# Performance work log

Hardware: AMD Instinct MI355X
Metric: run time of the kernel (lower is better)

The kernel has to match this reference:

```python
import jax, jax.numpy as jnp
import numpy as np

N = 100000      # nodes
E = 1600000     # edges (avg degree 16)
IN = 128        # in_channels
H = 128         # hidden_channels
EPS = 1e-5      # BatchNorm eps


def setup_inputs() -> dict:
    key = jax.random.key(0)
    ks = jax.random.split(key, 10)
    x = jax.random.normal(ks[0], (N, IN), jnp.float32)
    edge_index = jax.random.randint(ks[1], (2, E), 0, N, dtype=jnp.int32)

    def lin(k, i, o):
        return jax.random.normal(k, (i, o), jnp.float32) * (1.0 / np.sqrt(i))

    d2 = 2 * H
    return {
        "x": x, "edge_index": edge_index,
        # SAGEConv 1: 128 -> 128
        "w1l": lin(ks[2], IN, H), "w1r": lin(ks[3], IN, H), "b1": jnp.zeros((H,), jnp.float32),
        "g1": jnp.ones((H,), jnp.float32), "be1": jnp.zeros((H,), jnp.float32),
        "m1": jnp.zeros((H,), jnp.float32), "v1": jnp.ones((H,), jnp.float32),
        # SAGEConv 2: 128 -> 256
        "w2l": lin(ks[4], H, d2), "w2r": lin(ks[5], H, d2), "b2": jnp.zeros((d2,), jnp.float32),
        "g2": jnp.ones((d2,), jnp.float32), "be2": jnp.zeros((d2,), jnp.float32),
        "m2": jnp.zeros((d2,), jnp.float32), "v2": jnp.ones((d2,), jnp.float32),
        # SAGEConv 3: 256 -> 256
        "w3l": lin(ks[6], d2, d2), "w3r": lin(ks[7], d2, d2), "b3": jnp.zeros((d2,), jnp.float32),
        "g3": jnp.ones((d2,), jnp.float32), "be3": jnp.zeros((d2,), jnp.float32),
        "m3": jnp.zeros((d2,), jnp.float32), "v3": jnp.ones((d2,), jnp.float32),
    }


def _sage_conv(x, src, dst, wl, wr, b):
    # PyG SAGEConv (mean aggr): out = mean_{j in N(i)} x_j @ W_l + x_i @ W_r + b
    agg = jax.ops.segment_sum(x[src], dst, num_segments=N)          # [N, d_in]
    deg = jax.ops.segment_sum(jnp.ones((src.shape[0],), x.dtype), dst, num_segments=N)
    mean = agg / jnp.maximum(deg, 1.0)[:, None]
    return mean @ wl + x @ wr + b


def _bn(x, g, b, m, v):
    # BatchNorm1d in eval mode (running stats); dropout is a no-op in eval
    return (x - m) * jax.lax.rsqrt(v + EPS) * g + b


def reference(x, edge_index,
              w1l, w1r, b1, g1, be1, m1, v1,
              w2l, w2r, b2, g2, be2, m2, v2,
              w3l, w3r, b3, g3, be3, m3, v3):
    src, dst = edge_index[0], edge_index[1]
    h = _bn(jax.nn.relu(_sage_conv(x, src, dst, w1l, w1r, b1)), g1, be1, m1, v1)
    h = _bn(jax.nn.relu(_sage_conv(h, src, dst, w2l, w2r, b2)), g2, be2, m2, v2)
    h = _bn(jax.nn.relu(_sage_conv(h, src, dst, w3l, w3r, b3)), g3, be3, m3, v3)
    return h  # [N, 2*H]
```

## Files before the change

### kernel.cpp

```cpp
#include <hip/hip_runtime.h>

#define NNODES 100000
#define NEDGES 1600000
#define EPSV 1e-5f

#define NB   391
#define BCAP 4608
#define EPB  4096

#define PART_BLKS 391
#define CVT_BLKS  12500
#define WT_BLKS   896

typedef __attribute__((ext_vector_type(8))) short bf16x8;
typedef __attribute__((ext_vector_type(4))) float f32x4;
typedef __attribute__((ext_vector_type(2))) float f32x2;

#if defined(__has_builtin)
#  if __has_builtin(__builtin_amdgcn_cvt_pk_f32_fp8) && __has_builtin(__builtin_amdgcn_cvt_pk_fp8_f32)
#    define HAS_FP8_CVT 1
#  endif
#endif
#ifndef HAS_FP8_CVT
#  define HAS_FP8_CVT 0
#endif

__device__ __forceinline__ ushort f2bf(float f) {
    union { float f; uint u; } c; c.f = f;
    uint u = c.u;
    return (ushort)((u + 0x7fffu + ((u >> 16) & 1u)) >> 16);
}
__device__ __forceinline__ uint pack2(float f0, float f1) {
    return (uint)f2bf(f0) | ((uint)f2bf(f1) << 16);
}

#if !HAS_FP8_CVT
__device__ __forceinline__ float fp8_dec1(uint b) {
    uint e = (b >> 3) & 0xFu, m = b & 7u, s = b >> 7;
    union { uint u; float f; } c;
    c.u = e ? ((s << 31) | ((e + 120u) << 23) | (m << 20)) : (s << 31);
    return c.f;
}
__device__ __forceinline__ uint fp8_enc1(float x) {
    union { float f; uint u; } c; c.f = x;
    uint u = c.u, s = u >> 31;
    float ax = fabsf(x);
    if (ax < 0.015625f) return s << 7;
    if (ax > 448.0f)    return (s << 7) | 0x7Eu;
    u = u + 0x7FFFFu + ((u >> 20) & 1u);
    uint e = ((u >> 23) & 0xFFu) - 120u;
    uint m = (u >> 20) & 7u;
    if (e > 15u) return (s << 7) | 0x7Eu;
    return (s << 7) | (e << 3) | m;
}
#endif

__device__ __forceinline__ void accf8p(f32x2* a, uint2 v) {
#if HAS_FP8_CVT
    a[0] += __builtin_amdgcn_cvt_pk_f32_fp8((int)v.x, false);
    a[1] += __builtin_amdgcn_cvt_pk_f32_fp8((int)v.x, true);
    a[2] += __builtin_amdgcn_cvt_pk_f32_fp8((int)v.y, false);
    a[3] += __builtin_amdgcn_cvt_pk_f32_fp8((int)v.y, true);
#else
    a[0] += (f32x2){fp8_dec1(v.x & 0xFFu), fp8_dec1((v.x >> 8) & 0xFFu)};
    a[1] += (f32x2){fp8_dec1((v.x >> 16) & 0xFFu), fp8_dec1(v.x >> 24)};
    a[2] += (f32x2){fp8_dec1(v.y & 0xFFu), fp8_dec1((v.y >> 8) & 0xFFu)};
    a[3] += (f32x2){fp8_dec1((v.y >> 16) & 0xFFu), fp8_dec1(v.y >> 24)};
#endif
}

__device__ __forceinline__ uint f2fp8(float f) {
#if HAS_FP8_CVT
    return ((uint)__builtin_amdgcn_cvt_pk_fp8_f32(f, f, 0, false)) & 0xFFu;
#else
    return fp8_enc1(f);
#endif
}

__device__ __forceinline__ uint packf8_4(float f0, float f1, float f2, float f3) {
#if HAS_FP8_CVT
    int r = 0;
    r = __builtin_amdgcn_cvt_pk_fp8_f32(f0, f1, r, false);
    r = __builtin_amdgcn_cvt_pk_fp8_f32(f2, f3, r, true);
    return (uint)r;
#else
    return fp8_enc1(f0) | (fp8_enc1(f1) << 8) | (fp8_enc1(f2) << 16) | (fp8_enc1(f3) << 24);
#endif
}

__device__ __forceinline__ void load_lds16(const ushort* g, ushort* l) {
    __builtin_amdgcn_global_load_lds(
        (const __attribute__((address_space(1))) void*)g,
        (__attribute__((address_space(3))) void*)l,
        16, 0, 0);
}

__global__ __launch_bounds__(256) void pre_kernel(
    const int* __restrict__ src, const int* __restrict__ dst,
    int* __restrict__ cursor, uint2* __restrict__ pairs, int E,
    const float* __restrict__ x, ushort* __restrict__ xbf,
    unsigned char* __restrict__ xf8, int n4,
    const float* __restrict__ w1l, const float* __restrict__ w1r,
    const float* __restrict__ w2l, const float* __restrict__ w2r,
    const float* __restrict__ w3l, const float* __restrict__ w3r,
    ushort* __restrict__ t1l, ushort* __restrict__ t1r,
    ushort* __restrict__ t2l, ushort* __restrict__ t2r,
    ushort* __restrict__ t3l, ushort* __restrict__ t3r)
{
    const int t = threadIdx.x;

    if (blockIdx.x < PART_BLKS) {
        __shared__ int lcnt[NB];
        __shared__ int lbase[NB];
        for (int i = t; i < NB; i += 256) lcnt[i] = 0;
        __syncthreads();

        const int base = blockIdx.x * EPB;
        const int lim  = min(base + EPB, E);

        for (int e = base + t; e < lim; e += 256)
            atomicAdd(&lcnt[((unsigned)dst[e]) >> 8], 1);
        __syncthreads();

        for (int i = t; i < NB; i += 256) {
            int c = lcnt[i];
            lbase[i] = c ? atomicAdd(&cursor[i], c) : 0;
            lcnt[i] = 0;
        }
        __syncthreads();

        for (int e = base + t; e < lim; e += 256) {
            int d = dst[e];
            int b = ((unsigned)d) >> 8;
            int p = lbase[b] + atomicAdd(&lcnt[b], 1);
            if (p < BCAP) pairs[(size_t)b * BCAP + p] = make_uint2((uint)src[e], (uint)d);
        }
    } else if (blockIdx.x < PART_BLKS + CVT_BLKS) {
        int i = (blockIdx.x - PART_BLKS) * 256 + t;
        if (i < n4) {
            float4 v = ((const float4*)x)[i];
            ushort4 o;
            o.x = f2bf(v.x); o.y = f2bf(v.y); o.z = f2bf(v.z); o.w = f2bf(v.w);
            ((ushort4*)xbf)[i] = o;
            ((uint*)xf8)[i] = packf8_4(v.x, v.y, v.z, v.w);
        }
    } else {
        int idx = (blockIdx.x - PART_BLKS - CVT_BLKS) * 256 + t;
        const float* w; ushort* wt; int K, Nout, i;
        if      (idx <  16384) { w = w1l; wt = t1l; K = 128; Nout = 128; i = idx; }
        else if (idx <  32768) { w = w1r; wt = t1r; K = 128; Nout = 128; i = idx - 16384; }
        else if (idx <  65536) { w = w2l; wt = t2l; K = 128; Nout = 256; i = idx - 32768; }
        else if (idx <  98304) { w = w2r; wt = t2r; K = 128; Nout = 256; i = idx - 65536; }
        else if (idx < 163840) { w = w3l; wt = t3l; K = 256; Nout = 256; i = idx - 98304; }
        else if (idx < 229376) { w = w3r; wt = t3r; K = 256; Nout = 256; i = idx - 163840; }
        else return;
        int k = i / Nout, n = i - k * Nout;
        wt[(size_t)n * K + k] = f2bf(w[i]);
    }
}

__global__ __launch_bounds__(512) void bscan_kernel(const int* __restrict__ cursor,
                                                    int* __restrict__ colBase)
{
    __shared__ int s[512];
    int t = threadIdx.x;
    int v = (t < NB) ? min(cursor[t], BCAP) : 0;
    s[t] = v;
    __syncthreads();
    #pragma unroll
    for (int off = 1; off < 512; off <<= 1) {
        int a = (t >= off) ? s[t - off] : 0;
        __syncthreads();
        s[t] += a;
        __syncthreads();
    }
    if (t < NB) colBase[t] = s[t] - v;
}

__global__ __launch_bounds__(256) void csr_fin_kernel(
    const uint2* __restrict__ pairs, const int* __restrict__ cursor,
    const int* __restrict__ colBase, uint2* __restrict__ meta,
    int* __restrict__ col, int n)
{
    __shared__ int lcnt[256];
    __shared__ int lofs[256];
    const int b = blockIdx.x;
    const int t = threadIdx.x;
    const int ecnt  = min(cursor[b], BCAP);
    const int cbase = colBase[b];
    const uint2* __restrict__ pp = pairs + (size_t)b * BCAP;

    lcnt[t] = 0;
    __syncthreads();
    for (int e = t; e < ecnt; e += 256)
        atomicAdd(&lcnt[pp[e].y & 255u], 1);
    __syncthreads();

    const int v = lcnt[t];
    lofs[t] = v;
    __syncthreads();
    #pragma unroll
    for (int off = 1; off < 256; off <<= 1) {
        int a = (t >= off) ? lofs[t - off] : 0;
        __syncthreads();
        lofs[t] += a;
        __syncthreads();
    }
    const int excl = lofs[t] - v;

    const int node = (b << 8) + t;
    if (node < n)
        meta[node] = make_uint2((uint)(cbase + excl), (uint)v);
    __syncthreads();
    lcnt[t] = excl;
    __syncthreads();

    for (int e = t; e < ecnt; e += 256) {
        uint2 pr = pp[e];
        int p = cbase + atomicAdd(&lcnt[pr.y & 255u], 1);
        col[p] = (int)pr.x;
    }
}

template<int D>
__global__ __launch_bounds__(256) void gather_f8(
    const unsigned char* __restrict__ x, const uint2* __restrict__ meta,
    const int* __restrict__ col, ushort* __restrict__ agg, int n)
{
    constexpr int TPN = D / 8;
    constexpr int NPB = 256 / TPN;
    const int node = blockIdx.x * NPB + threadIdx.x / TPN;
    const int lane = threadIdx.x % TPN;
    if (node >= n) return;

    const uint2 m  = meta[node];
    const int  c   = (int)m.y;
    int        e   = (int)m.x;
    const int  end = e + c;
    const uint boff = (uint)lane * 8u;

    f32x2 a[4];
    #pragma unroll
    for (int i = 0; i < 4; ++i) a[i] = (f32x2)0.0f;

    while (e + 15 < end) {
        uint2 r[16];
        #pragma unroll
        for (int i = 0; i < 16; ++i)
            r[i] = *(const uint2*)(x + (uint)col[e + i] * (uint)D + boff);
        #pragma unroll
        for (int i = 0; i < 16; ++i) accf8p(a, r[i]);
        e += 16;
    }
    if (e + 7 < end) {
        uint2 r[8];
        #pragma unroll
        for (int i = 0; i < 8; ++i)
            r[i] = *(const uint2*)(x + (uint)col[e + i] * (uint)D + boff);
        #pragma unroll
        for (int i = 0; i < 8; ++i) accf8p(a, r[i]);
        e += 8;
    }
    for (; e + 1 < end; e += 2) {
        uint2 v0 = *(const uint2*)(x + (uint)col[e]     * (uint)D + boff);
        uint2 v1 = *(const uint2*)(x + (uint)col[e + 1] * (uint)D + boff);
        accf8p(a, v0); accf8p(a, v1);
    }
    if (e < end) {
        uint2 v = *(const uint2*)(x + (uint)col[e] * (uint)D + boff);
        accf8p(a, v);
    }

    const float inv = 1.0f / fmaxf((float)c, 1.0f);
    uint4 o;
    o.x = pack2(a[0][0] * inv, a[0][1] * inv);
    o.y = pack2(a[1][0] * inv, a[1][1] * inv);
    o.z = pack2(a[2][0] * inv, a[2][1] * inv);
    o.w = pack2(a[3][0] * inv, a[3][1] * inv);
    ((uint4*)agg)[(size_t)node * TPN + lane] = o;
}

template<int DIN, int DOUT, bool OUTF32, bool WRITE8>
__global__ __launch_bounds__(256) void mfma_layer(
    const ushort* __restrict__ xin, const ushort* __restrict__ agg,
    const ushort* __restrict__ wlT, const ushort* __restrict__ wrT,
    const float* __restrict__ bias, const float* __restrict__ gamma,
    const float* __restrict__ beta, const float* __restrict__ rmean,
    const float* __restrict__ rvar, void* __restrict__ outp,
    unsigned char* __restrict__ out8, int M)
{
    constexpr int BM = 128, BN = 128, BK = 64;
    constexpr int NBY = DOUT / BN;
    __shared__ ushort As[BM * BK];
    __shared__ ushort Bs[BN * BK];

    const int tid  = threadIdx.x;
    const int lane = tid & 63;
    const int wid  = tid >> 6;
    const int wm   = (wid & 1) * 64;
    const int wn   = (wid >> 1) * 64;
    const int lr   = lane & 15;
    const int quad = lane >> 4;

    const int row0 = (blockIdx.x / NBY) * BM;
    const int col0 = (blockIdx.x % NBY) * BN;

    f32x4 acc[4][4] = {};

    const int srow = tid >> 3;
    const int schk = (tid & 7) ^ (srow & 7);

    #pragma unroll
    for (int phase = 0; phase < 2; ++phase) {
        const ushort* __restrict__ A = phase ? xin : agg;
        const ushort* __restrict__ W = phase ? wrT : wlT;

        for (int k0 = 0; k0 < DIN; k0 += BK) {
            __syncthreads();
            #pragma unroll
            for (int r = 0; r < 4; ++r) {
                const int row = srow + r * 32;
                int gra = row0 + row; gra = gra < M ? gra : M - 1;
                load_lds16(A + (size_t)gra * DIN + k0 + schk * 8,
                           &As[(r * 256 + tid) * 8]);
                load_lds16(W + (size_t)(col0 + row) * DIN + k0 + schk * 8,
                           &Bs[(r * 256 + tid) * 8]);
            }
            __syncthreads();

            #pragma unroll
            for (int sub = 0; sub < 2; ++sub) {
                bf16x8 af[4], bf[4];
                #pragma unroll
                for (int t = 0; t < 4; ++t) {
                    const int ra = wm + t * 16 + lr;
                    const int rb = wn + t * 16 + lr;
                    const int ca = ((sub << 2) | quad) ^ (ra & 7);
                    const int cb = ((sub << 2) | quad) ^ (rb & 7);
                    af[t] = *(const bf16x8*)&As[ra * BK + ca * 8];
                    bf[t] = *(const bf16x8*)&Bs[rb * BK + cb * 8];
                }
                #pragma unroll
                for (int mt = 0; mt < 4; ++mt)
                    #pragma unroll
                    for (int nt = 0; nt < 4; ++nt)
                        acc[mt][nt] = __builtin_amdgcn_mfma_f32_16x16x32_bf16(
                            af[mt], bf[nt], acc[mt][nt], 0, 0, 0);
            }
        }
    }

    float bj[4], sj[4], mj[4], bej[4];
    #pragma unroll
    for (int nt = 0; nt < 4; ++nt) {
        int gc = col0 + wn + nt * 16 + lr;
        bj[nt]  = bias[gc];
        sj[nt]  = rsqrtf(rvar[gc] + EPSV) * gamma[gc];
        mj[nt]  = rmean[gc];
        bej[nt] = beta[gc];
    }
    #pragma unroll
    for (int mt = 0; mt < 4; ++mt) {
        #pragma unroll
        for (int r = 0; r < 4; ++r) {
            int grow = row0 + wm + mt * 16 + quad * 4 + r;
            if (grow < M) {
                #pragma unroll
                for (int nt = 0; nt < 4; ++nt) {
                    int gc = col0 + wn + nt * 16 + lr;
                    float h = acc[mt][nt][r] + bj[nt];
                    h = fmaxf(h, 0.0f);
                    h = (h - mj[nt]) * sj[nt] + bej[nt];
                    if (OUTF32) ((float*)outp)[(size_t)grow * DOUT + gc] = h;
                    else        ((ushort*)outp)[(size_t)grow * DOUT + gc] = f2bf(h);
                    if (WRITE8) out8[(size_t)grow * DOUT + gc] = (unsigned char)f2fp8(h);
                }
            }
        }
    }
}

extern "C" void kernel_launch(void* const* d_in, const int* in_sizes, int n_in,
                              void* d_out, int out_size, void* d_ws, size_t ws_size,
                              hipStream_t stream) {
    const int N = NNODES;
    const int E = NEDGES;

    const float* x   = (const float*)d_in[0];
    const int*   ei  = (const int*)d_in[1];
    const int*   src = ei;
    const int*   dst = ei + E;

    const float* w1l = (const float*)d_in[2];
    const float* w1r = (const float*)d_in[3];
    const float* b1  = (const float*)d_in[4];
    const float* g1  = (const float*)d_in[5];
    const float* be1 = (const float*)d_in[6];
    const float* m1  = (const float*)d_in[7];
    const float* v1  = (const float*)d_in[8];

    const float* w2l = (const float*)d_in[9];
    const float* w2r = (const float*)d_in[10];
    const float* b2  = (const float*)d_in[11];
    const float* g2  = (const float*)d_in[12];
    const float* be2 = (const float*)d_in[13];
    const float* m2  = (const float*)d_in[14];
    const float* v2  = (const float*)d_in[15];

    const float* w3l = (const float*)d_in[16];
    const float* w3r = (const float*)d_in[17];
    const float* b3  = (const float*)d_in[18];
    const float* g3  = (const float*)d_in[19];
    const float* be3 = (const float*)d_in[20];
    const float* m3  = (const float*)d_in[21];
    const float* v3  = (const float*)d_in[22];

    float* out = (float*)d_out;

    char*   wp      = (char*)d_ws;
    uint2*  meta    = (uint2*)wp;   wp += (size_t)N * sizeof(uint2);
    int*    cursor  = (int*)wp;     wp += 512 * sizeof(int);
    int*    colBase = (int*)wp;     wp += 512 * sizeof(int);
    int*    col     = (int*)wp;     wp += (size_t)E * sizeof(int);
    uint2*  pairs   = (uint2*)wp;   wp += (size_t)NB * BCAP * sizeof(uint2);
    ushort* xbf     = (ushort*)wp;  wp += (size_t)N * 128 * sizeof(ushort);
    ushort* h1      = (ushort*)wp;  wp += (size_t)N * 128 * sizeof(ushort);
    ushort* h2      = (ushort*)wp;  wp += (size_t)N * 256 * sizeof(ushort);
    ushort* aggb    = (ushort*)wp;  wp += (size_t)N * 256 * sizeof(ushort);
    unsigned char* h2f8 = (unsigned char*)wp; wp += (size_t)N * 256;
    ushort* w1lT    = (ushort*)wp;  wp += 128 * 128 * sizeof(ushort);
    ushort* w1rT    = (ushort*)wp;  wp += 128 * 128 * sizeof(ushort);
    ushort* w2lT    = (ushort*)wp;  wp += 256 * 128 * sizeof(ushort);
    ushort* w2rT    = (ushort*)wp;  wp += 256 * 128 * sizeof(ushort);
    ushort* w3lT    = (ushort*)wp;  wp += 256 * 256 * sizeof(ushort);
    ushort* w3rT    = (ushort*)wp;

    unsigned char* xf8  = (unsigned char*)h2;
    unsigned char* h1f8 = (unsigned char*)pairs;

    hipMemsetAsync(cursor, 0, 512 * sizeof(int), stream);
    pre_kernel<<<PART_BLKS + CVT_BLKS + WT_BLKS, 256, 0, stream>>>(
        src, dst, cursor, pairs, E,
        x, xbf, xf8, N * 128 / 4,
        w1l, w1r, w2l, w2r, w3l, w3r,
        w1lT, w1rT, w2lT, w2rT, w3lT, w3rT);
    bscan_kernel<<<1, 512, 0, stream>>>(cursor, colBase);
    csr_fin_kernel<<<NB, 256, 0, stream>>>(pairs, cursor, colBase, meta, col, N);

    const int nrb = (N + 127) / 128;

    gather_f8<128><<<(N + 15) / 16, 256, 0, stream>>>(xf8, meta, col, aggb, N);
    mfma_layer<128, 128, false, true><<<nrb * 1, 256, 0, stream>>>(
        xbf, aggb, w1lT, w1rT, b1, g1, be1, m1, v1, h1, h1f8, N);

    gather_f8<128><<<(N + 15) / 16, 256, 0, stream>>>(h1f8, meta, col, aggb, N);
    mfma_layer<128, 256, false, true><<<nrb * 2, 256, 0, stream>>>(
        h1, aggb, w2lT, w2rT, b2, g2, be2, m2, v2, h2, h2f8, N);

    gather_f8<256><<<(N + 7) / 8, 256, 0, stream>>>(h2f8, meta, col, aggb, N);
    mfma_layer<256, 256, true, false><<<nrb * 2, 256, 0, stream>>>(
        h2, aggb, w3lT, w3rT, b3, g3, be3, m3, v3, out, nullptr, N);
}
```

Before: 475.4 us.

## Replace bucketed two-pass CSR build with global atomic count-scan-scatter

Replaces the bucket-partition plus per-bucket local sort CSR construction with a per-node global atomic degree count, a three-stage prefix scan, and an atomic-cursor scatter of source indices. This drops the intermediate pairs buffer and the BCAP capacity limit, which could drop edges when a bucket overflowed. In exchange it uses many more global atomics on contended addresses, adds extra kernel launches, and makes neighbour order within each row nondeterministic.

```diff
diff --git a/kernel.cpp b/kernel.cpp
--- a/kernel.cpp
+++ b/kernel.cpp
@@ -5,7 +5,6 @@
 #define EPSV 1e-5f
 
 #define NB   391
-#define BCAP 4608
 #define EPB  4096
 
 #define PART_BLKS 391
@@ -96,8 +95,7 @@
 }
 
 __global__ __launch_bounds__(256) void pre_kernel(
-    const int* __restrict__ src, const int* __restrict__ dst,
-    int* __restrict__ cursor, uint2* __restrict__ pairs, int E,
+    const int* __restrict__ dst, int* __restrict__ cnt, int E,
     const float* __restrict__ x, ushort* __restrict__ xbf,
     unsigned char* __restrict__ xf8, int n4,
     const float* __restrict__ w1l, const float* __restrict__ w1r,
@@ -110,31 +108,10 @@
     const int t = threadIdx.x;
 
     if (blockIdx.x < PART_BLKS) {
-        __shared__ int lcnt[NB];
-        __shared__ int lbase[NB];
-        for (int i = t; i < NB; i += 256) lcnt[i] = 0;
-        __syncthreads();
-
         const int base = blockIdx.x * EPB;
         const int lim  = min(base + EPB, E);
-
         for (int e = base + t; e < lim; e += 256)
-            atomicAdd(&lcnt[((unsigned)dst[e]) >> 8], 1);
-        __syncthreads();
-
-        for (int i = t; i < NB; i += 256) {
-            int c = lcnt[i];
-            lbase[i] = c ? atomicAdd(&cursor[i], c) : 0;
-            lcnt[i] = 0;
-        }
-        __syncthreads();
-
-        for (int e = base + t; e < lim; e += 256) {
-            int d = dst[e];
-            int b = ((unsigned)d) >> 8;
-            int p = lbase[b] + atomicAdd(&lcnt[b], 1);
-            if (p < BCAP) pairs[(size_t)b * BCAP + p] = make_uint2((uint)src[e], (uint)d);
-        }
+            atomicAdd(&cnt[dst[e]], 1);
     } else if (blockIdx.x < PART_BLKS + CVT_BLKS) {
         int i = (blockIdx.x - PART_BLKS) * 256 + t;
         if (i < n4) {
@@ -159,12 +136,33 @@
     }
 }
 
-__global__ __launch_bounds__(512) void bscan_kernel(const int* __restrict__ cursor,
-                                                    int* __restrict__ colBase)
+__global__ __launch_bounds__(256) void scanA_kernel(
+    const int* __restrict__ cnt, uint2* __restrict__ meta,
+    int* __restrict__ bsum, int n)
+{
+    __shared__ int s[256];
+    const int b = blockIdx.x, t = threadIdx.x;
+    const int node = (b << 8) + t;
+    const int v = (node < n) ? cnt[node] : 0;
+    s[t] = v;
+    __syncthreads();
+    #pragma unroll
+    for (int off = 1; off < 256; off <<= 1) {
+        int a = (t >= off) ? s[t - off] : 0;
+        __syncthreads();
+        s[t] += a;
+        __syncthreads();
+    }
+    if (node < n) meta[node] = make_uint2((uint)(s[t] - v), (uint)v);
+    if (t == 255) bsum[b] = s[255];
+}
+
+__global__ __launch_bounds__(512) void scanB_kernel(const int* __restrict__ bsum,
+                                                    int* __restrict__ bbase)
 {
     __shared__ int s[512];
     int t = threadIdx.x;
-    int v = (t < NB) ? min(cursor[t], BCAP) : 0;
+    int v = (t < NB) ? bsum[t] : 0;
     s[t] = v;
     __syncthreads();
     #pragma unroll
@@ -174,51 +172,31 @@
         s[t] += a;
         __syncthreads();
     }
-    if (t < NB) colBase[t] = s[t] - v;
-}
-
-__global__ __launch_bounds__(256) void csr_fin_kernel(
-    const uint2* __restrict__ pairs, const int* __restrict__ cursor,
-    const int* __restrict__ colBase, uint2* __restrict__ meta,
-    int* __restrict__ col, int n)
-{
-    __shared__ int lcnt[256];
-    __shared__ int lofs[256];
-    const int b = blockIdx.x;
-    const int t = threadIdx.x;
-    const int ecnt  = min(cursor[b], BCAP);
-    const int cbase = colBase[b];
-    const uint2* __restrict__ pp = pairs + (size_t)b * BCAP;
-
-    lcnt[t] = 0;
-    __syncthreads();
-    for (int e = t; e < ecnt; e += 256)
-        atomicAdd(&lcnt[pp[e].y & 255u], 1);
-    __syncthreads();
-
-    const int v = lcnt[t];
-    lofs[t] = v;
-    __syncthreads();
-    #pragma unroll
-    for (int off = 1; off < 256; off <<= 1) {
-        int a = (t >= off) ? lofs[t - off] : 0;
-        __syncthreads();
-        lofs[t] += a;
-        __syncthreads();
-    }
-    const int excl = lofs[t] - v;
-
-    const int node = (b << 8) + t;
-    if (node < n)
-        meta[node] = make_uint2((uint)(cbase + excl), (uint)v);
-    __syncthreads();
-    lcnt[t] = excl;
-    __syncthreads();
-
-    for (int e = t; e < ecnt; e += 256) {
-        uint2 pr = pp[e];
-        int p = cbase + atomicAdd(&lcnt[pr.y & 255u], 1);
-        col[p] = (int)pr.x;
+    if (t < NB) bbase[t] = s[t] - v;
+}
+
+__global__ __launch_bounds__(256) void scanC_kernel(
+    uint2* __restrict__ meta, const int* __restrict__ bbase,
+    int* __restrict__ cursor, int n)
+{
+    const int node = blockIdx.x * 256 + threadIdx.x;
+    if (node < n) {
+        uint2 m = meta[node];
+        uint beg = m.x + (uint)bbase[node >> 8];
+        meta[node] = make_uint2(beg, m.y);
+        cursor[node] = (int)beg;
+    }
+}
+
+__global__ __launch_bounds__(256) void scatter_kernel(
+    const int* __restrict__ src, const int* __restrict__ dst,
+    int* __restrict__ cursor, int* __restrict__ col, int E)
+{
+    const int base = blockIdx.x * EPB;
+    const int lim  = min(base + EPB, E);
+    for (int e = base + threadIdx.x; e < lim; e += 256) {
+        int p = atomicAdd(&cursor[dst[e]], 1);
+        col[p] = src[e];
     }
 }
 
@@ -419,15 +397,16 @@
 
     char*   wp      = (char*)d_ws;
     uint2*  meta    = (uint2*)wp;   wp += (size_t)N * sizeof(uint2);
-    int*    cursor  = (int*)wp;     wp += 512 * sizeof(int);
-    int*    colBase = (int*)wp;     wp += 512 * sizeof(int);
+    int*    cnt     = (int*)wp;     wp += (size_t)N * sizeof(int);
+    int*    bsum    = (int*)wp;     wp += 512 * sizeof(int);
+    int*    bbase   = (int*)wp;     wp += 512 * sizeof(int);
     int*    col     = (int*)wp;     wp += (size_t)E * sizeof(int);
-    uint2*  pairs   = (uint2*)wp;   wp += (size_t)NB * BCAP * sizeof(uint2);
     ushort* xbf     = (ushort*)wp;  wp += (size_t)N * 128 * sizeof(ushort);
     ushort* h1      = (ushort*)wp;  wp += (size_t)N * 128 * sizeof(ushort);
     ushort* h2      = (ushort*)wp;  wp += (size_t)N * 256 * sizeof(ushort);
     ushort* aggb    = (ushort*)wp;  wp += (size_t)N * 256 * sizeof(ushort);
     unsigned char* h2f8 = (unsigned char*)wp; wp += (size_t)N * 256;
+    unsigned char* h1f8 = (unsigned char*)wp; wp += (size_t)N * 128;
     ushort* w1lT    = (ushort*)wp;  wp += 128 * 128 * sizeof(ushort);
     ushort* w1rT    = (ushort*)wp;  wp += 128 * 128 * sizeof(ushort);
     ushort* w2lT    = (ushort*)wp;  wp += 256 * 128 * sizeof(ushort);
@@ -435,17 +414,18 @@
     ushort* w3lT    = (ushort*)wp;  wp += 256 * 256 * sizeof(ushort);
     ushort* w3rT    = (ushort*)wp;
 
-    unsigned char* xf8  = (unsigned char*)h2;
-    unsigned char* h1f8 = (unsigned char*)pairs;
-
-    hipMemsetAsync(cursor, 0, 512 * sizeof(int), stream);
+    unsigned char* xf8 = (unsigned char*)h2;
+
+    hipMemsetAsync(cnt, 0, (size_t)N * sizeof(int), stream);
     pre_kernel<<<PART_BLKS + CVT_BLKS + WT_BLKS, 256, 0, stream>>>(
-        src, dst, cursor, pairs, E,
+        dst, cnt, E,
         x, xbf, xf8, N * 128 / 4,
         w1l, w1r, w2l, w2r, w3l, w3r,
         w1lT, w1rT, w2lT, w2rT, w3lT, w3rT);
-    bscan_kernel<<<1, 512, 0, stream>>>(cursor, colBase);
-    csr_fin_kernel<<<NB, 256, 0, stream>>>(pairs, cursor, colBase, meta, col, N);
+    scanA_kernel<<<NB, 256, 0, stream>>>(cnt, meta, bsum, N);
+    scanB_kernel<<<1, 512, 0, stream>>>(bsum, bbase);
+    scanC_kernel<<<NB, 256, 0, stream>>>(meta, bbase, cnt, N);
+    scatter_kernel<<<PART_BLKS, 256, 0, stream>>>(src, dst, cnt, col, E);
 
     const int nrb = (N + 127) / 128;
 
```

After: 582.4 us. 1.23x slower.
